# Performance work log

Measured on AMD Instinct MI355X. Metric: run time of the kernel, lower is better.

Reference implementation:

```python
import jax, jax.numpy as jnp
import numpy as np

SIGNAL_LENGTH = 2048
BASE_STEP_SIZE = 0.01
MAX_ITERATIONS = 15
STEP_DECAY = 0.9
MIN_STEP = 1e-4
POS_TOL = 1e-4
EPS_SCALES = (0.001, 0.003, 0.01)
EPS_WEIGHTS = (0.5, 0.3, 0.2)


def setup_inputs() -> dict:
    key = jax.random.key(0)
    k1, k2 = jax.random.split(key)
    batch = 32768
    initial_predictions = jax.random.uniform(k1, (batch, 3), dtype=jnp.float32)
    signals = jax.random.normal(k2, (batch, SIGNAL_LENGTH), dtype=jnp.float32)
    return {"initial_predictions": initial_predictions, "signals": signals}


def _sample(signals, positions):
    # signals: [B, L], positions in [0,1]: [B, P] -> values [B, P]
    L = SIGNAL_LENGTH
    p = jnp.clip(positions * (L - 1), 0.0, float(L - 1))
    il = jnp.clip(jnp.floor(p).astype(jnp.int32), 0, L - 1)
    ir = jnp.clip(jnp.ceil(p).astype(jnp.int32), 0, L - 1)
    vl = jnp.take_along_axis(signals, il, axis=1)
    vr = jnp.take_along_axis(signals, ir, axis=1)
    wr = p - il.astype(p.dtype)
    return (1.0 - wr) * vl + wr * vr


def _grads_and_curvs(signals, positions):
    g_acc = 0.0
    c_acc = 0.0
    for eps, w in zip(EPS_SCALES, EPS_WEIGHTS):
        pc = jnp.clip(positions, eps, 1.0 - eps)
        v = _sample(signals, pc)
        vl = _sample(signals, pc - eps)
        vr = _sample(signals, pc + eps)
        g_acc = g_acc + w * (vr - vl) / (2.0 * eps)
        c_acc = c_acc + w * (vr + vl - 2.0 * v) / (eps * eps)
    return g_acc, jnp.clip(c_acc, -1000.0, 1000.0)


def _refine(initial_predictions, signals):
    positions = initial_predictions
    prev_positions = positions
    best_positions = positions
    best_values = _sample(signals, positions)
    step_size0 = jnp.asarray(BASE_STEP_SIZE, dtype=positions.dtype)
    done0 = jnp.asarray(False)

    def body(carry, it):
        positions, prev, best_pos, best_val, step_size, done = carry
        g, c = _grads_and_curvs(signals, positions)
        step = -g / (jnp.abs(c) + 1e-6)
        max_step = 0.2 * (STEP_DECAY ** it)
        step = jnp.clip(step, -max_step, max_step)
        new_pos = jnp.clip(positions + step_size * step, 0.0, 1.0)
        cur_val = _sample(signals, new_pos)
        # NOTE: original code sets best_positions = positions.clone() then
        # where(mask, positions, best_positions) -> best_positions == new_pos always
        new_best_pos = new_pos
        new_best_val = jnp.where(cur_val > best_val, cur_val, best_val)
        pos_change = jnp.max(jnp.abs(new_pos - prev))
        stop = (pos_change < POS_TOL) | (step_size < MIN_STEP)
        new_step = jnp.where(stop, step_size, step_size * STEP_DECAY)
        new_prev = jnp.where(stop, prev, new_pos)
        sel = lambda n, o: jnp.where(done, o, n)
        carry = (sel(new_pos, positions), sel(new_prev, prev),
                 sel(new_best_pos, best_pos), sel(new_best_val, best_val),
                 jnp.where(done, step_size, new_step), done | stop)
        return carry, None

    its = jnp.arange(MAX_ITERATIONS, dtype=positions.dtype)
    carry0 = (positions, prev_positions, best_positions, best_values, step_size0, done0)
    (_, _, best_positions, _, _, _), _ = jax.lax.scan(body, carry0, its)
    return best_positions


def reference(initial_predictions, signals):
    if signals.ndim == 3:
        signals = signals[:, 0, :]
    return _refine(initial_predictions, signals)
```

## Files before the change

### kernel.cpp

```cpp
#include <hip/hip_runtime.h>

#define SIG_LEN 2048
#define LM1F 2047.0f
#define N_ITER 15

__device__ __forceinline__ float sample_sig(const float* __restrict__ sig, float q) {
    float p = __fmul_rn(q, LM1F);
    p = fminf(fmaxf(p, 0.0f), LM1F);
    float fl = floorf(p);
    float cl = ceilf(p);
    int il = (int)fl;
    int ir = (int)cl;
    float wr = __fsub_rn(p, fl);
    float vl = sig[il];
    float vr = sig[ir];
    return __fadd_rn(__fmul_rn(__fsub_rn(1.0f, wr), vl), __fmul_rn(wr, vr));
}

__device__ __forceinline__ void fd_contrib(const float* __restrict__ sig, float pos,
                                           float eps, float one_m_eps, float w,
                                           float two_eps, float eps_sq,
                                           float& g, float& c) {
    float pc = fminf(fmaxf(pos, eps), one_m_eps);
    float v  = sample_sig(sig, pc);
    float vl = sample_sig(sig, __fsub_rn(pc, eps));
    float vr = sample_sig(sig, __fadd_rn(pc, eps));
    g = __fadd_rn(g, __fmul_rn(w, __fsub_rn(vr, vl)) / two_eps);
    float t = __fsub_rn(__fadd_rn(vr, vl), __fmul_rn(2.0f, v));
    c = __fadd_rn(c, __fmul_rn(w, t) / eps_sq);
}

__global__ __launch_bounds__(256) void refine_kernel(
    const float* __restrict__ init,
    const float* __restrict__ signals,
    float* __restrict__ out, int n)
{
    int idx = blockIdx.x * blockDim.x + threadIdx.x;
    if (idx >= n) return;

    int row = idx / 3;
    const float* __restrict__ sig = signals + (size_t)row * SIG_LEN;

    float pos = init[idx];
    float ss = 0.01f;

    const float ms_tab[N_ITER] = {
        0.2f, 0.18f, 0.162f, 0.1458f, 0.13122f,
        0.118098f, 0.1062882f, 0.09565938f, 0.086093442f, 0.0774840978f,
        0.06973568802f, 0.062762119218f, 0.0564859072962f, 0.05083731656658f,
        0.045753584909922f
    };

    #pragma unroll
    for (int it = 0; it < N_ITER; ++it) {
        float g = 0.0f, c = 0.0f;
        fd_contrib(sig, pos, 0.001f, 0.999f, 0.5f, 0.002f, 1e-06f, g, c);
        fd_contrib(sig, pos, 0.003f, 0.997f, 0.3f, 0.006f, 9e-06f, g, c);
        fd_contrib(sig, pos, 0.01f,  0.99f,  0.2f, 0.02f,  1e-04f, g, c);

        c = fminf(fmaxf(c, -1000.0f), 1000.0f);
        float step = (-g) / __fadd_rn(fabsf(c), 1e-06f);
        float ms = ms_tab[it];
        step = fminf(fmaxf(step, -ms), ms);
        pos = fminf(fmaxf(__fadd_rn(pos, __fmul_rn(ss, step)), 0.0f), 1.0f);
        ss = __fmul_rn(ss, 0.9f);
    }

    out[idx] = pos;
}

extern "C" void kernel_launch(void* const* d_in, const int* in_sizes, int n_in,
                              void* d_out, int out_size, void* d_ws, size_t ws_size,
                              hipStream_t stream) {
    const float* init    = (const float*)d_in[0];
    const float* signals = (const float*)d_in[1];
    float* out = (float*)d_out;

    int n = out_size;
    int block = 256;
    int grid = (n + block - 1) / block;
    refine_kernel<<<grid, block, 0, stream>>>(init, signals, out, n);
}
```

Baseline: 357.6 us.

## Stage per-task signal windows into LDS before refinement iterations

Each thread's sampling region is bounded: the position moves by at most 0.01 per iteration with decaying step size, so the total drift is below about 0.1 in normalized units, roughly 40 samples. The kernel now loads a 96-sample window around each task's starting position into shared memory with cooperative loads, then runs all iterations against LDS instead of scattered global reads. Block size drops to 128 and the bounds check is removed, assuming n is a multiple of 128. The window bound is a correctness risk if positions ever leave it, and the large shared allocation (about 50KB per block) limits occupancy.

```diff
diff --git a/kernel.cpp b/kernel.cpp
--- a/kernel.cpp
+++ b/kernel.cpp
@@ -3,45 +3,66 @@
 #define SIG_LEN 2048
 #define LM1F 2047.0f
 #define N_ITER 15
+#define TPB 128
+#define WIN 96
+#define WPAD 97
 
-__device__ __forceinline__ float sample_sig(const float* __restrict__ sig, float q) {
+__device__ __forceinline__ float sample_lds(const float* __restrict__ w, float q) {
     float p = __fmul_rn(q, LM1F);
     p = fminf(fmaxf(p, 0.0f), LM1F);
     float fl = floorf(p);
-    float cl = ceilf(p);
     int il = (int)fl;
-    int ir = (int)cl;
+    int inc = (p > fl) ? 1 : 0;
     float wr = __fsub_rn(p, fl);
-    float vl = sig[il];
-    float vr = sig[ir];
+    float vl = w[il];
+    float vr = w[il + inc];
     return __fadd_rn(__fmul_rn(__fsub_rn(1.0f, wr), vl), __fmul_rn(wr, vr));
 }
 
-__device__ __forceinline__ void fd_contrib(const float* __restrict__ sig, float pos,
-                                           float eps, float one_m_eps, float w,
+__device__ __forceinline__ void fd_contrib(const float* __restrict__ w, float pos,
+                                           float eps, float one_m_eps, float wgt,
                                            float two_eps, float eps_sq,
                                            float& g, float& c) {
     float pc = fminf(fmaxf(pos, eps), one_m_eps);
-    float v  = sample_sig(sig, pc);
-    float vl = sample_sig(sig, __fsub_rn(pc, eps));
-    float vr = sample_sig(sig, __fadd_rn(pc, eps));
-    g = __fadd_rn(g, __fmul_rn(w, __fsub_rn(vr, vl)) / two_eps);
+    float v  = sample_lds(w, pc);
+    float vl = sample_lds(w, __fsub_rn(pc, eps));
+    float vr = sample_lds(w, __fadd_rn(pc, eps));
+    g = __fadd_rn(g, __fmul_rn(wgt, __fsub_rn(vr, vl)) / two_eps);
     float t = __fsub_rn(__fadd_rn(vr, vl), __fmul_rn(2.0f, v));
-    c = __fadd_rn(c, __fmul_rn(w, t) / eps_sq);
+    c = __fadd_rn(c, __fmul_rn(wgt, t) / eps_sq);
 }
 
-__global__ __launch_bounds__(256) void refine_kernel(
+__global__ __launch_bounds__(TPB) void refine_kernel(
     const float* __restrict__ init,
     const float* __restrict__ signals,
-    float* __restrict__ out, int n)
+    float* __restrict__ out)
 {
-    int idx = blockIdx.x * blockDim.x + threadIdx.x;
-    if (idx >= n) return;
+    __shared__ float win[TPB * WPAD];
+    __shared__ int   wbase[TPB];
 
-    int row = idx / 3;
-    const float* __restrict__ sig = signals + (size_t)row * SIG_LEN;
+    const int tid   = threadIdx.x;
+    const int task0 = blockIdx.x * TPB;
+    const int task  = task0 + tid;
 
-    float pos = init[idx];
+    const float p0 = init[task];
+    float pp = fminf(fmaxf(__fmul_rn(p0, LM1F), 0.0f), LM1F);
+    int base = (int)floorf(pp) - 47;
+    base = min(max(base, 0), SIG_LEN - WIN);
+    wbase[tid] = base;
+    __syncthreads();
+
+    #pragma unroll 4
+    for (int k = tid; k < TPB * WIN; k += TPB) {
+        int t = k / WIN;
+        int e = k - t * WIN;
+        int row = (task0 + t) / 3;
+        win[t * WPAD + e] = signals[(size_t)row * SIG_LEN + (wbase[t] + e)];
+    }
+    __syncthreads();
+
+    const float* __restrict__ w = &win[tid * WPAD] - base;
+
+    float pos = p0;
     float ss = 0.01f;
 
     const float ms_tab[N_ITER] = {
@@ -54,9 +75,9 @@
     #pragma unroll
     for (int it = 0; it < N_ITER; ++it) {
         float g = 0.0f, c = 0.0f;
-        fd_contrib(sig, pos, 0.001f, 0.999f, 0.5f, 0.002f, 1e-06f, g, c);
-        fd_contrib(sig, pos, 0.003f, 0.997f, 0.3f, 0.006f, 9e-06f, g, c);
-        fd_contrib(sig, pos, 0.01f,  0.99f,  0.2f, 0.02f,  1e-04f, g, c);
+        fd_contrib(w, pos, 0.001f, 0.999f, 0.5f, 0.002f, 1e-06f, g, c);
+        fd_contrib(w, pos, 0.003f, 0.997f, 0.3f, 0.006f, 9e-06f, g, c);
+        fd_contrib(w, pos, 0.01f,  0.99f,  0.2f, 0.02f,  1e-04f, g, c);
 
         c = fminf(fmaxf(c, -1000.0f), 1000.0f);
         float step = (-g) / __fadd_rn(fabsf(c), 1e-06f);
@@ -66,7 +87,7 @@
         ss = __fmul_rn(ss, 0.9f);
     }
 
-    out[idx] = pos;
+    out[task] = pos;
 }
 
 extern "C" void kernel_launch(void* const* d_in, const int* in_sizes, int n_in,
@@ -77,7 +98,6 @@
     float* out = (float*)d_out;
 
     int n = out_size;
-    int block = 256;
-    int grid = (n + block - 1) / block;
-    refine_kernel<<<grid, block, 0, stream>>>(init, signals, out, n);
+    int grid = n / TPB;
+    refine_kernel<<<grid, TPB, 0, stream>>>(init, signals, out);
 }
```

Result: faster. 321.2 us (-10.2%).
